# Performance work log

Hardware: AMD Instinct MI355X
Metric: run time of the kernel (lower is better)

Reference implementation:

```python
import jax, jax.numpy as jnp
import numpy as np

B, T = 1024, 1024
D_IN, UNITS, WIDTH, DEPTH, D_OUT = 6, 64, 128, 3, 6
START = UNITS + D_IN  # concat([x_normed, h]) width
EPS = 1e-8


def _xavier(key, fin, fout):
    lim = float(np.sqrt(6.0 / (fin + fout)))
    return jax.random.uniform(key, (fin, fout), minval=-lim, maxval=lim, dtype=jnp.float32)


def setup_inputs() -> dict:
    key = jax.random.key(0)
    ks = jax.random.split(key, 12)
    d = {
        "x": jax.random.normal(ks[0], (B, T, D_IN), dtype=jnp.float32),
        "init_F": jax.random.normal(ks[1], (B, 2 + UNITS), dtype=jnp.float32) * 0.1,
    }
    dims = [START] + [WIDTH] * DEPTH
    for i in range(DEPTH):
        d[f"qb1_w{i}"] = _xavier(ks[2 + 2 * i], dims[i], dims[i + 1])
        d[f"qb1_b{i}"] = jnp.zeros((dims[i + 1],), dtype=jnp.float32)
        d[f"qb2_w{i}"] = _xavier(ks[3 + 2 * i], dims[i], dims[i + 1])
        d[f"qb2_b{i}"] = jnp.zeros((dims[i + 1],), dtype=jnp.float32)
    d["wa"] = _xavier(ks[8], WIDTH, UNITS)
    d["ba"] = jnp.zeros((UNITS,), dtype=jnp.float32)
    d["wb"] = _xavier(ks[9], WIDTH, UNITS)
    d["bb"] = jnp.zeros((UNITS,), dtype=jnp.float32)
    # fc_out bias is frozen at zero in the original -> weight only
    d["wout"] = _xavier(ks[10], UNITS, D_OUT)
    return d


def reference(x, init_F,
              qb1_w0, qb1_b0, qb2_w0, qb2_b0,
              qb1_w1, qb1_b1, qb2_w1, qb2_b1,
              qb1_w2, qb1_b2, qb2_w2, qb2_b2,
              wa, ba, wb, bb, wout):
    layers = ((qb1_w0, qb1_b0, qb2_w0, qb2_b0),
              (qb1_w1, qb1_b1, qb2_w1, qb2_b1),
              (qb1_w2, qb1_b2, qb2_w2, qb2_b2))
    h0 = init_F[:, 2:2 + UNITS]  # [B, UNITS]

    def step(h, xt):  # xt: [B, D_IN], h: [B, UNITS]
        norm = jnp.sqrt(jnp.sum(xt * xt, axis=1, keepdims=True))  # [B,1]
        xn = xt / (norm + EPS)
        c = jnp.concatenate([xn, h], axis=1)  # [B, START]
        for i, (w1, b1, w2, b2) in enumerate(layers):
            x1 = c @ w1 + b1
            x2 = c @ w2 + b2
            if i < DEPTH - 1:
                x1 = jnp.tanh(x1)
                x2 = jnp.tanh(x2)
            c = x1 * x2
        g = jnp.tanh(c)
        alpha = jnp.exp(g @ wa + ba)          # [B, UNITS]
        beta = jnp.tanh(g @ wb + bb)          # [B, UNITS]
        h_new = jnp.exp(-alpha * norm) * (h - beta) + beta
        return h_new, (h_new @ wout, alpha)

    _, (outs, alphas) = jax.lax.scan(step, h0, jnp.swapaxes(x, 0, 1))
    # outs: [T,B,D_OUT], alphas: [T,B,UNITS] -> batch-major
    return jnp.swapaxes(outs, 0, 1), jnp.swapaxes(alphas, 0, 1)
```

## Files before the change

### kernel.cpp

```cpp
#include <hip/hip_runtime.h>
#include <stdint.h>
#include <stddef.h>

#define NB 1024
#define TB 1024
#define D_IN 6
#define UNITS 64
#define WIDTH 128
#define DOUT 6
#define EPSF 1e-8f
#define SPB 16
#define LDK0 108
#define LDK 140

typedef _Float16 v8h __attribute__((ext_vector_type(8)));
typedef float v4f __attribute__((ext_vector_type(4)));

#define MFMAH(A,Bf,C) __builtin_amdgcn_mfma_f32_16x16x32_f16((A),(Bf),(C),0,0,0)

#define BARRIER_LDS() asm volatile("s_waitcnt lgkmcnt(0)\n\ts_barrier" ::: "memory")

#define C2L2E  2.8853900817779268f
#define L2E    1.4426950408889634f
#define NEGL2E (-1.4426950408889634f)

__device__ __forceinline__ float rcp_fast(float x){ return __builtin_amdgcn_rcpf(x); }

__device__ __forceinline__ float tanh_from_arg(float a2){
  float u = __builtin_amdgcn_exp2f(a2);
  return fmaf(-2.0f, rcp_fast(u + 1.0f), 1.0f);
}
__device__ __forceinline__ float tanh_e(float x){ return tanh_from_arg(x * C2L2E); }

__device__ __forceinline__ void make_frag1(const float* vals, v8h& hv){
  #pragma unroll
  for (int j = 0; j < 8; j++) hv[j] = (_Float16)vals[j];
}
__device__ __forceinline__ void make_frag2(const float* vals, v8h& hv, v8h& lv){
  #pragma unroll
  for (int j = 0; j < 8; j++){
    _Float16 h = (_Float16)vals[j];
    hv[j] = h;
    lv[j] = (_Float16)(vals[j] - (float)h);
  }
}

__global__ __launch_bounds__(512, 2) void lmsc_kernel(
    const float* __restrict__ x, const float* __restrict__ initF,
    const float* __restrict__ w10, const float* __restrict__ b10,
    const float* __restrict__ w20, const float* __restrict__ b20,
    const float* __restrict__ w11, const float* __restrict__ b11,
    const float* __restrict__ w21, const float* __restrict__ b21,
    const float* __restrict__ w12, const float* __restrict__ b12,
    const float* __restrict__ w22, const float* __restrict__ b22,
    const float* __restrict__ wa, const float* __restrict__ ba,
    const float* __restrict__ wb, const float* __restrict__ bb,
    const float* __restrict__ wo,
    float* __restrict__ outs, float* __restrict__ alph)
{
  __shared__ __attribute__((aligned(16))) _Float16 c0[2][SPB*LDK0];
  __shared__ __attribute__((aligned(16))) _Float16 cP[SPB*LDK];
  __shared__ __attribute__((aligned(16))) _Float16 cQ[SPB*LDK];
  __shared__ __attribute__((aligned(16))) _Float16 cG[SPB*LDK];
  __shared__ __attribute__((aligned(16))) float nrm[2][SPB];

  const int tid = threadIdx.x;
  const int wv = tid >> 6;
  const int ln = tid & 63;
  const int mn = ln & 15;
  const int qd = ln >> 4;
  const int q8 = qd * 8;
  const int n  = wv * 16 + mn;
  const int sgbase = (int)blockIdx.x * SPB;

  float tmp[8];

  v8h B0[3][2];
  #pragma unroll
  for (int kf = 0; kf < 3; kf++)
    #pragma unroll
    for (int br = 0; br < 2; br++){
      const float* W = br ? w20 : w10;
      #pragma unroll
      for (int j = 0; j < 8; j++){
        int k = kf*32 + q8 + j;
        int r = (k < 6) ? k : ((k >= 8 && k < 72) ? (k - 2) : -1);
        tmp[j] = (r >= 0) ? W[r*WIDTH + n] : 0.0f;
      }
      make_frag1(tmp, B0[kf][br]);
    }

  v8h B1[4][2], B2[4][2];
  #pragma unroll
  for (int kf = 0; kf < 4; kf++)
    #pragma unroll
    for (int br = 0; br < 2; br++){
      const float* W = br ? w21 : w11;
      #pragma unroll
      for (int j = 0; j < 8; j++)
        tmp[j] = W[(kf*32 + q8 + j)*WIDTH + n];
      make_frag1(tmp, B1[kf][br]);
      const float* V = br ? w22 : w12;
      #pragma unroll
      for (int j = 0; j < 8; j++)
        tmp[j] = V[(kf*32 + q8 + j)*WIDTH + n];
      make_frag1(tmp, B2[kf][br]);
    }

  const int u = (wv & 3) * 16 + mn;
  v8h Bah[4], Bal[4], Bbh[4];
  #pragma unroll
  for (int kf = 0; kf < 4; kf++){
    #pragma unroll
    for (int j = 0; j < 8; j++)
      tmp[j] = wa[(kf*32 + q8 + j)*UNITS + u];
    make_frag2(tmp, Bah[kf], Bal[kf]);
    #pragma unroll
    for (int j = 0; j < 8; j++)
      tmp[j] = wb[(kf*32 + q8 + j)*UNITS + u];
    make_frag1(tmp, Bbh[kf]);
  }
  const float bsa = ba[u];
  const float bsb = bb[u];

  v8h Woh0, Woh1;
  #pragma unroll
  for (int j = 0; j < 8; j++)
    tmp[j] = (mn < DOUT) ? wo[(q8 + j)*DOUT + mn] : 0.0f;
  make_frag1(tmp, Woh0);
  #pragma unroll
  for (int j = 0; j < 8; j++)
    tmp[j] = (mn < DOUT) ? wo[(32 + q8 + j)*DOUT + mn] : 0.0f;
  make_frag1(tmp, Woh1);

  const float bs0a = b10[n], bs0b = b20[n];
  const float bs1a = b11[n], bs1b = b21[n];
  const float bs2a = b12[n], bs2b = b22[n];
  const float e0a = bs0a * C2L2E, e0b = bs0b * C2L2E;
  const float e1a = bs1a * C2L2E, e1b = bs1b * C2L2E;

  float* alp  = alph + ((size_t)(sgbase + qd*4) * TB) * UNITS + u;
  float* outp = outs + ((size_t)(sgbase + qd*4) * TB) * DOUT + mn;

  for (int i = tid; i < 2*SPB*LDK0; i += 512) c0[0][i] = (_Float16)0.0f;
  __syncthreads();

  float hreg[4];
  if (wv < 4){
    #pragma unroll
    for (int r = 0; r < 4; r++){
      int s = qd*4 + r;
      float v = initF[(size_t)(sgbase + s)*(2 + UNITS) + 2 + u];
      hreg[r] = v;
      c0[0][s*LDK0 + 8 + u] = (_Float16)v;
    }
  }
  float xv0=0, xv1=0, xv2=0, xv3=0, xv4=0, xv5=0;
  if (wv == 4 && ln < 16){
    const float* xp = x + (size_t)(sgbase + ln)*TB*D_IN;
    float a0=xp[0], a1=xp[1], a2=xp[2], a3=xp[3], a4=xp[4], a5=xp[5];
    float nv = sqrtf(a0*a0 + a1*a1 + a2*a2 + a3*a3 + a4*a4 + a5*a5);
    nrm[0][ln] = nv * NEGL2E;
    float inv = 1.0f / (nv + EPSF);
    c0[0][ln*LDK0 + 0] = (_Float16)(a0*inv);
    c0[0][ln*LDK0 + 1] = (_Float16)(a1*inv);
    c0[0][ln*LDK0 + 2] = (_Float16)(a2*inv);
    c0[0][ln*LDK0 + 3] = (_Float16)(a3*inv);
    c0[0][ln*LDK0 + 4] = (_Float16)(a4*inv);
    c0[0][ln*LDK0 + 5] = (_Float16)(a5*inv);
    xv0 = xp[6]; xv1 = xp[7]; xv2 = xp[8]; xv3 = xp[9]; xv4 = xp[10]; xv5 = xp[11];
  }
  __syncthreads();

  auto wout_phase = [&](const _Float16* cb, int tt){
    v8h ah0 = *(const v8h*)(cb + mn*LDK0 + 8 + q8);
    v8h ah1 = *(const v8h*)(cb + mn*LDK0 + 40 + q8);
    v4f acc = {0.f, 0.f, 0.f, 0.f};
    acc = MFMAH(ah0, Woh0, acc);
    acc = MFMAH(ah1, Woh1, acc);
    if (mn < DOUT){
      #pragma unroll
      for (int r = 0; r < 4; r++)
        outp[(size_t)r*TB*DOUT + (size_t)tt*DOUT] = acc[r];
    }
  };

  for (int t = 0; t < TB; t++){
    const int p = t & 1;
    const _Float16* c0r = c0[p];
    _Float16* c0w = c0[p ^ 1];

    {
      v8h ah[3];
      #pragma unroll
      for (int kf = 0; kf < 3; kf++)
        ah[kf] = *(const v8h*)(c0r + mn*LDK0 + kf*32 + q8);
      v4f acc0 = {0.f, 0.f, 0.f, 0.f};
      v4f acc1 = {0.f, 0.f, 0.f, 0.f};
      #pragma unroll
      for (int kf = 0; kf < 3; kf++){
        acc0 = MFMAH(ah[kf], B0[kf][0], acc0);
        acc1 = MFMAH(ah[kf], B0[kf][1], acc1);
      }
      #pragma unroll
      for (int r = 0; r < 4; r++){
        float t0 = tanh_from_arg(fmaf(acc0[r], C2L2E, e0a));
        float t1 = tanh_from_arg(fmaf(acc1[r], C2L2E, e0b));
        cP[(qd*4 + r)*LDK + n] = (_Float16)(t0 * t1);
      }
    }
    BARRIER_LDS();

    {
      v8h ah[4];
      #pragma unroll
      for (int kf = 0; kf < 4; kf++)
        ah[kf] = *(const v8h*)(cP + mn*LDK + kf*32 + q8);
      v4f acc0 = {0.f, 0.f, 0.f, 0.f};
      v4f acc1 = {0.f, 0.f, 0.f, 0.f};
      #pragma unroll
      for (int kf = 0; kf < 4; kf++){
        acc0 = MFMAH(ah[kf], B1[kf][0], acc0);
        acc1 = MFMAH(ah[kf], B1[kf][1], acc1);
      }
      #pragma unroll
      for (int r = 0; r < 4; r++){
        float t0 = tanh_from_arg(fmaf(acc0[r], C2L2E, e1a));
        float t1 = tanh_from_arg(fmaf(acc1[r], C2L2E, e1b));
        cQ[(qd*4 + r)*LDK + n] = (_Float16)(t0 * t1);
      }
    }
    BARRIER_LDS();

    {
      v8h ah[4];
      #pragma unroll
      for (int kf = 0; kf < 4; kf++)
        ah[kf] = *(const v8h*)(cQ + mn*LDK + kf*32 + q8);
      v4f acc0 = {bs2a, bs2a, bs2a, bs2a};
      v4f acc1 = {bs2b, bs2b, bs2b, bs2b};
      #pragma unroll
      for (int kf = 0; kf < 4; kf++){
        acc0 = MFMAH(ah[kf], B2[kf][0], acc0);
        acc1 = MFMAH(ah[kf], B2[kf][1], acc1);
      }
      #pragma unroll
      for (int r = 0; r < 4; r++)
        cG[(qd*4 + r)*LDK + n] = (_Float16)tanh_e(acc0[r] * acc1[r]);
    }
    BARRIER_LDS();

    if (wv < 4){
      v8h gh[4];
      #pragma unroll
      for (int kf = 0; kf < 4; kf++)
        gh[kf] = *(const v8h*)(cG + mn*LDK + kf*32 + q8);
      v4f pA0 = {bsa, bsa, bsa, bsa};
      v4f pA1 = {0.f, 0.f, 0.f, 0.f};
      v4f pB  = {bsb, bsb, bsb, bsb};
      #pragma unroll
      for (int kf = 0; kf < 2; kf++){
        pA0 = MFMAH(gh[kf], Bah[kf], pA0);
        pA0 = MFMAH(gh[kf], Bal[kf], pA0);
        pA1 = MFMAH(gh[kf+2], Bah[kf+2], pA1);
        pA1 = MFMAH(gh[kf+2], Bal[kf+2], pA1);
        pB  = MFMAH(gh[2*kf],   Bbh[2*kf],   pB);
        pB  = MFMAH(gh[2*kf+1], Bbh[2*kf+1], pB);
      }
      #pragma unroll
      for (int r = 0; r < 4; r++){
        int s = qd*4 + r;
        float m = nrm[p][s];
        float alpha = __builtin_amdgcn_exp2f((pA0[r] + pA1[r]) * L2E);
        float beta  = tanh_e(pB[r]);
        float dec   = __builtin_amdgcn_exp2f(alpha * m);
        float h = fmaf(dec, hreg[r] - beta, beta);
        hreg[r] = h;
        c0w[s*LDK0 + 8 + u] = (_Float16)h;
        alp[(size_t)r*TB*UNITS] = alpha;
      }
      alp += UNITS;
    } else if (wv == 7){
      if (t > 0) wout_phase(c0r, t - 1);
    } else if (wv == 4 && ln < 16){
      float nv2 = sqrtf(xv0*xv0 + xv1*xv1 + xv2*xv2 + xv3*xv3 + xv4*xv4 + xv5*xv5);
      nrm[p ^ 1][ln] = nv2 * NEGL2E;
      float inv = 1.0f / (nv2 + EPSF);
      c0w[ln*LDK0 + 0] = (_Float16)(xv0*inv);
      c0w[ln*LDK0 + 1] = (_Float16)(xv1*inv);
      c0w[ln*LDK0 + 2] = (_Float16)(xv2*inv);
      c0w[ln*LDK0 + 3] = (_Float16)(xv3*inv);
      c0w[ln*LDK0 + 4] = (_Float16)(xv4*inv);
      c0w[ln*LDK0 + 5] = (_Float16)(xv5*inv);
      int tn = t + 2; if (tn > TB - 1) tn = TB - 1;
      const float* xp = x + ((size_t)(sgbase + ln)*TB + (size_t)tn)*D_IN;
      xv0 = xp[0]; xv1 = xp[1]; xv2 = xp[2]; xv3 = xp[3]; xv4 = xp[4]; xv5 = xp[5];
    }
    BARRIER_LDS();
  }

  if (wv == 7) wout_phase(c0[TB & 1], TB - 1);
}

extern "C" void kernel_launch(void* const* d_in, const int* in_sizes, int n_in,
                              void* d_out, int out_size, void* d_ws, size_t ws_size,
                              hipStream_t stream) {
  const float* x    = (const float*)d_in[0];
  const float* iF   = (const float*)d_in[1];
  const float* w10  = (const float*)d_in[2];
  const float* b10  = (const float*)d_in[3];
  const float* w20  = (const float*)d_in[4];
  const float* b20  = (const float*)d_in[5];
  const float* w11  = (const float*)d_in[6];
  const float* b11  = (const float*)d_in[7];
  const float* w21  = (const float*)d_in[8];
  const float* b21  = (const float*)d_in[9];
  const float* w12  = (const float*)d_in[10];
  const float* b12  = (const float*)d_in[11];
  const float* w22  = (const float*)d_in[12];
  const float* b22  = (const float*)d_in[13];
  const float* wa   = (const float*)d_in[14];
  const float* ba   = (const float*)d_in[15];
  const float* wb   = (const float*)d_in[16];
  const float* bb   = (const float*)d_in[17];
  const float* wo   = (const float*)d_in[18];

  float* outs = (float*)d_out;
  float* alph = outs + (size_t)NB*TB*DOUT;

  lmsc_kernel<<<NB/SPB, 512, 0, stream>>>(x, iF,
      w10, b10, w20, b20, w11, b11, w21, b21, w12, b12, w22, b22,
      wa, ba, wb, bb, wo, outs, alph);
}
```

Before: 2.379 ms.

## Process two 16-sequence tiles per block, sharing weight fragments across tiles

Doubles sequences per block from 16 to 32 by splitting the block's state into two 16-row tiles. Every wave now runs interleaved MFMA chains for both tiles against the same register-resident weight fragments. All eight waves take part in the alpha/beta/h update phase, and the output projection is split between waves 1 and 6. The aim is to hide per-step MFMA and barrier latency with independent work and to reuse weights. The cost is half as many blocks on an already underfilled GPU, and roughly twice the work on each block's serial time-step path.

```diff
diff --git a/kernel.cpp b/kernel.cpp
--- a/kernel.cpp
+++ b/kernel.cpp
@@ -9,7 +9,8 @@
 #define WIDTH 128
 #define DOUT 6
 #define EPSF 1e-8f
-#define SPB 16
+#define SPB 32
+#define T16 16
 #define LDK0 108
 #define LDK 140
 
@@ -58,11 +59,11 @@
     const float* __restrict__ wo,
     float* __restrict__ outs, float* __restrict__ alph)
 {
-  __shared__ __attribute__((aligned(16))) _Float16 c0[2][SPB*LDK0];
-  __shared__ __attribute__((aligned(16))) _Float16 cP[SPB*LDK];
-  __shared__ __attribute__((aligned(16))) _Float16 cQ[SPB*LDK];
-  __shared__ __attribute__((aligned(16))) _Float16 cG[SPB*LDK];
-  __shared__ __attribute__((aligned(16))) float nrm[2][SPB];
+  __shared__ __attribute__((aligned(16))) _Float16 c0[2][2][T16*LDK0];
+  __shared__ __attribute__((aligned(16))) _Float16 cP[2][T16*LDK];
+  __shared__ __attribute__((aligned(16))) _Float16 cQ[2][T16*LDK];
+  __shared__ __attribute__((aligned(16))) _Float16 cG[2][T16*LDK];
+  __shared__ __attribute__((aligned(16))) float nrm[2][2][T16];
 
   const int tid = threadIdx.x;
   const int wv = tid >> 6;
@@ -72,6 +73,7 @@
   const int q8 = qd * 8;
   const int n  = wv * 16 + mn;
   const int sgbase = (int)blockIdx.x * SPB;
+  const int dtile = wv >> 2;
 
   float tmp[8];
 
@@ -133,41 +135,44 @@
     tmp[j] = (mn < DOUT) ? wo[(32 + q8 + j)*DOUT + mn] : 0.0f;
   make_frag1(tmp, Woh1);
 
-  const float bs0a = b10[n], bs0b = b20[n];
-  const float bs1a = b11[n], bs1b = b21[n];
   const float bs2a = b12[n], bs2b = b22[n];
-  const float e0a = bs0a * C2L2E, e0b = bs0b * C2L2E;
-  const float e1a = bs1a * C2L2E, e1b = bs1b * C2L2E;
-
-  float* alp  = alph + ((size_t)(sgbase + qd*4) * TB) * UNITS + u;
-  float* outp = outs + ((size_t)(sgbase + qd*4) * TB) * DOUT + mn;
-
-  for (int i = tid; i < 2*SPB*LDK0; i += 512) c0[0][i] = (_Float16)0.0f;
+  const float e0a = b10[n] * C2L2E, e0b = b20[n] * C2L2E;
+  const float e1a = b11[n] * C2L2E, e1b = b21[n] * C2L2E;
+
+  float* alp  = alph + ((size_t)(sgbase + dtile*T16 + qd*4) * TB) * UNITS + u;
+  const int wtile = (wv == 1) ? 0 : 1;
+  float* outp = outs + ((size_t)(sgbase + wtile*T16 + qd*4) * TB) * DOUT + mn;
+
+  {
+    _Float16* cz = &c0[0][0][0];
+    for (int i = tid; i < 2*2*T16*LDK0; i += 512) cz[i] = (_Float16)0.0f;
+  }
   __syncthreads();
 
   float hreg[4];
-  if (wv < 4){
-    #pragma unroll
-    for (int r = 0; r < 4; r++){
-      int s = qd*4 + r;
-      float v = initF[(size_t)(sgbase + s)*(2 + UNITS) + 2 + u];
-      hreg[r] = v;
-      c0[0][s*LDK0 + 8 + u] = (_Float16)v;
-    }
-  }
+  #pragma unroll
+  for (int r = 0; r < 4; r++){
+    int s = qd*4 + r;
+    float v = initF[(size_t)(sgbase + dtile*T16 + s)*(2 + UNITS) + 2 + u];
+    hreg[r] = v;
+    c0[0][dtile][s*LDK0 + 8 + u] = (_Float16)v;
+  }
+
   float xv0=0, xv1=0, xv2=0, xv3=0, xv4=0, xv5=0;
-  if (wv == 4 && ln < 16){
+  if (wv == 4 && ln < 32){
+    const int tl = ln >> 4, s = ln & 15;
     const float* xp = x + (size_t)(sgbase + ln)*TB*D_IN;
     float a0=xp[0], a1=xp[1], a2=xp[2], a3=xp[3], a4=xp[4], a5=xp[5];
     float nv = sqrtf(a0*a0 + a1*a1 + a2*a2 + a3*a3 + a4*a4 + a5*a5);
-    nrm[0][ln] = nv * NEGL2E;
+    nrm[0][tl][s] = nv * NEGL2E;
     float inv = 1.0f / (nv + EPSF);
-    c0[0][ln*LDK0 + 0] = (_Float16)(a0*inv);
-    c0[0][ln*LDK0 + 1] = (_Float16)(a1*inv);
-    c0[0][ln*LDK0 + 2] = (_Float16)(a2*inv);
-    c0[0][ln*LDK0 + 3] = (_Float16)(a3*inv);
-    c0[0][ln*LDK0 + 4] = (_Float16)(a4*inv);
-    c0[0][ln*LDK0 + 5] = (_Float16)(a5*inv);
+    _Float16* cw = &c0[0][tl][0];
+    cw[s*LDK0 + 0] = (_Float16)(a0*inv);
+    cw[s*LDK0 + 1] = (_Float16)(a1*inv);
+    cw[s*LDK0 + 2] = (_Float16)(a2*inv);
+    cw[s*LDK0 + 3] = (_Float16)(a3*inv);
+    cw[s*LDK0 + 4] = (_Float16)(a4*inv);
+    cw[s*LDK0 + 5] = (_Float16)(a5*inv);
     xv0 = xp[6]; xv1 = xp[7]; xv2 = xp[8]; xv3 = xp[9]; xv4 = xp[10]; xv5 = xp[11];
   }
   __syncthreads();
@@ -187,74 +192,95 @@
 
   for (int t = 0; t < TB; t++){
     const int p = t & 1;
-    const _Float16* c0r = c0[p];
-    _Float16* c0w = c0[p ^ 1];
+    const _Float16* c0r0 = c0[p][0];
+    const _Float16* c0r1 = c0[p][1];
+    _Float16* c0w0 = c0[p ^ 1][0];
+    _Float16* c0w1 = c0[p ^ 1][1];
 
     {
-      v8h ah[3];
-      #pragma unroll
-      for (int kf = 0; kf < 3; kf++)
-        ah[kf] = *(const v8h*)(c0r + mn*LDK0 + kf*32 + q8);
-      v4f acc0 = {0.f, 0.f, 0.f, 0.f};
-      v4f acc1 = {0.f, 0.f, 0.f, 0.f};
+      v8h a0[3], a1[3];
       #pragma unroll
       for (int kf = 0; kf < 3; kf++){
-        acc0 = MFMAH(ah[kf], B0[kf][0], acc0);
-        acc1 = MFMAH(ah[kf], B0[kf][1], acc1);
+        a0[kf] = *(const v8h*)(c0r0 + mn*LDK0 + kf*32 + q8);
+        a1[kf] = *(const v8h*)(c0r1 + mn*LDK0 + kf*32 + q8);
+      }
+      v4f q00 = {0,0,0,0}, q01 = {0,0,0,0}, q10 = {0,0,0,0}, q11 = {0,0,0,0};
+      #pragma unroll
+      for (int kf = 0; kf < 3; kf++){
+        q00 = MFMAH(a0[kf], B0[kf][0], q00);
+        q01 = MFMAH(a0[kf], B0[kf][1], q01);
+        q10 = MFMAH(a1[kf], B0[kf][0], q10);
+        q11 = MFMAH(a1[kf], B0[kf][1], q11);
       }
       #pragma unroll
       for (int r = 0; r < 4; r++){
-        float t0 = tanh_from_arg(fmaf(acc0[r], C2L2E, e0a));
-        float t1 = tanh_from_arg(fmaf(acc1[r], C2L2E, e0b));
-        cP[(qd*4 + r)*LDK + n] = (_Float16)(t0 * t1);
+        float t0 = tanh_from_arg(fmaf(q00[r], C2L2E, e0a));
+        float t1 = tanh_from_arg(fmaf(q01[r], C2L2E, e0b));
+        cP[0][(qd*4 + r)*LDK + n] = (_Float16)(t0 * t1);
+        float s0 = tanh_from_arg(fmaf(q10[r], C2L2E, e0a));
+        float s1 = tanh_from_arg(fmaf(q11[r], C2L2E, e0b));
+        cP[1][(qd*4 + r)*LDK + n] = (_Float16)(s0 * s1);
       }
     }
     BARRIER_LDS();
 
     {
-      v8h ah[4];
+      v8h a0[4], a1[4];
+      #pragma unroll
+      for (int kf = 0; kf < 4; kf++){
+        a0[kf] = *(const v8h*)(cP[0] + mn*LDK + kf*32 + q8);
+        a1[kf] = *(const v8h*)(cP[1] + mn*LDK + kf*32 + q8);
+      }
+      v4f q00 = {0,0,0,0}, q01 = {0,0,0,0}, q10 = {0,0,0,0}, q11 = {0,0,0,0};
+      #pragma unroll
+      for (int kf = 0; kf < 4; kf++){
+        q00 = MFMAH(a0[kf], B1[kf][0], q00);
+        q01 = MFMAH(a0[kf], B1[kf][1], q01);
+        q10 = MFMAH(a1[kf], B1[kf][0], q10);
+        q11 = MFMAH(a1[kf], B1[kf][1], q11);
+      }
+      #pragma unroll
+      for (int r = 0; r < 4; r++){
+        float t0 = tanh_from_arg(fmaf(q00[r], C2L2E, e1a));
+        float t1 = tanh_from_arg(fmaf(q01[r], C2L2E, e1b));
+        cQ[0][(qd*4 + r)*LDK + n] = (_Float16)(t0 * t1);
+        float s0 = tanh_from_arg(fmaf(q10[r], C2L2E, e1a));
+        float s1 = tanh_from_arg(fmaf(q11[r], C2L2E, e1b));
+        cQ[1][(qd*4 + r)*LDK + n] = (_Float16)(s0 * s1);
+      }
+    }
+    BARRIER_LDS();
+
+    {
+      v8h a0[4], a1[4];
+      #pragma unroll
+      for (int kf = 0; kf < 4; kf++){
+        a0[kf] = *(const v8h*)(cQ[0] + mn*LDK + kf*32 + q8);
+        a1[kf] = *(const v8h*)(cQ[1] + mn*LDK + kf*32 + q8);
+      }
+      v4f q00 = {bs2a,bs2a,bs2a,bs2a}, q01 = {bs2b,bs2b,bs2b,bs2b};
+      v4f q10 = {bs2a,bs2a,bs2a,bs2a}, q11 = {bs2b,bs2b,bs2b,bs2b};
+      #pragma unroll
+      for (int kf = 0; kf < 4; kf++){
+        q00 = MFMAH(a0[kf], B2[kf][0], q00);
+        q01 = MFMAH(a0[kf], B2[kf][1], q01);
+        q10 = MFMAH(a1[kf], B2[kf][0], q10);
+        q11 = MFMAH(a1[kf], B2[kf][1], q11);
+      }
+      #pragma unroll
+      for (int r = 0; r < 4; r++){
+        cG[0][(qd*4 + r)*LDK + n] = (_Float16)tanh_e(q00[r] * q01[r]);
+        cG[1][(qd*4 + r)*LDK + n] = (_Float16)tanh_e(q10[r] * q11[r]);
+      }
+    }
+    BARRIER_LDS();
+
+    {
+      const _Float16* cGt = cG[dtile];
+      v8h gh[4];
       #pragma unroll
       for (int kf = 0; kf < 4; kf++)
-        ah[kf] = *(const v8h*)(cP + mn*LDK + kf*32 + q8);
-      v4f acc0 = {0.f, 0.f, 0.f, 0.f};
-      v4f acc1 = {0.f, 0.f, 0.f, 0.f};
-      #pragma unroll
-      for (int kf = 0; kf < 4; kf++){
-        acc0 = MFMAH(ah[kf], B1[kf][0], acc0);
-        acc1 = MFMAH(ah[kf], B1[kf][1], acc1);
-      }
-      #pragma unroll
-      for (int r = 0; r < 4; r++){
-        float t0 = tanh_from_arg(fmaf(acc0[r], C2L2E, e1a));
-        float t1 = tanh_from_arg(fmaf(acc1[r], C2L2E, e1b));
-        cQ[(qd*4 + r)*LDK + n] = (_Float16)(t0 * t1);
-      }
-    }
-    BARRIER_LDS();
-
-    {
-      v8h ah[4];
-      #pragma unroll
-      for (int kf = 0; kf < 4; kf++)
-        ah[kf] = *(const v8h*)(cQ + mn*LDK + kf*32 + q8);
-      v4f acc0 = {bs2a, bs2a, bs2a, bs2a};
-      v4f acc1 = {bs2b, bs2b, bs2b, bs2b};
-      #pragma unroll
-      for (int kf = 0; kf < 4; kf++){
-        acc0 = MFMAH(ah[kf], B2[kf][0], acc0);
-        acc1 = MFMAH(ah[kf], B2[kf][1], acc1);
-      }
-      #pragma unroll
-      for (int r = 0; r < 4; r++)
-        cG[(qd*4 + r)*LDK + n] = (_Float16)tanh_e(acc0[r] * acc1[r]);
-    }
-    BARRIER_LDS();
-
-    if (wv < 4){
-      v8h gh[4];
-      #pragma unroll
-      for (int kf = 0; kf < 4; kf++)
-        gh[kf] = *(const v8h*)(cG + mn*LDK + kf*32 + q8);
+        gh[kf] = *(const v8h*)(cGt + mn*LDK + kf*32 + q8);
       v4f pA0 = {bsa, bsa, bsa, bsa};
       v4f pA1 = {0.f, 0.f, 0.f, 0.f};
       v4f pB  = {bsb, bsb, bsb, bsb};
@@ -267,31 +293,38 @@
         pB  = MFMAH(gh[2*kf],   Bbh[2*kf],   pB);
         pB  = MFMAH(gh[2*kf+1], Bbh[2*kf+1], pB);
       }
+      _Float16* c0wt = dtile ? c0w1 : c0w0;
+      const float* nr = nrm[p][dtile];
       #pragma unroll
       for (int r = 0; r < 4; r++){
         int s = qd*4 + r;
-        float m = nrm[p][s];
+        float m = nr[s];
         float alpha = __builtin_amdgcn_exp2f((pA0[r] + pA1[r]) * L2E);
         float beta  = tanh_e(pB[r]);
         float dec   = __builtin_amdgcn_exp2f(alpha * m);
         float h = fmaf(dec, hreg[r] - beta, beta);
         hreg[r] = h;
-        c0w[s*LDK0 + 8 + u] = (_Float16)h;
+        c0wt[s*LDK0 + 8 + u] = (_Float16)h;
         alp[(size_t)r*TB*UNITS] = alpha;
       }
       alp += UNITS;
-    } else if (wv == 7){
-      if (t > 0) wout_phase(c0r, t - 1);
-    } else if (wv == 4 && ln < 16){
+    }
+    if (wv == 1){
+      if (t > 0) wout_phase(c0r0, t - 1);
+    } else if (wv == 6){
+      if (t > 0) wout_phase(c0r1, t - 1);
+    } else if (wv == 4 && ln < 32){
+      const int tl = ln >> 4, s = ln & 15;
       float nv2 = sqrtf(xv0*xv0 + xv1*xv1 + xv2*xv2 + xv3*xv3 + xv4*xv4 + xv5*xv5);
-      nrm[p ^ 1][ln] = nv2 * NEGL2E;
+      nrm[p ^ 1][tl][s] = nv2 * NEGL2E;
       float inv = 1.0f / (nv2 + EPSF);
-      c0w[ln*LDK0 + 0] = (_Float16)(xv0*inv);
-      c0w[ln*LDK0 + 1] = (_Float16)(xv1*inv);
-      c0w[ln*LDK0 + 2] = (_Float16)(xv2*inv);
-      c0w[ln*LDK0 + 3] = (_Float16)(xv3*inv);
-      c0w[ln*LDK0 + 4] = (_Float16)(xv4*inv);
-      c0w[ln*LDK0 + 5] = (_Float16)(xv5*inv);
+      _Float16* cw = tl ? c0w1 : c0w0;
+      cw[s*LDK0 + 0] = (_Float16)(xv0*inv);
+      cw[s*LDK0 + 1] = (_Float16)(xv1*inv);
+      cw[s*LDK0 + 2] = (_Float16)(xv2*inv);
+      cw[s*LDK0 + 3] = (_Float16)(xv3*inv);
+      cw[s*LDK0 + 4] = (_Float16)(xv4*inv);
+      cw[s*LDK0 + 5] = (_Float16)(xv5*inv);
       int tn = t + 2; if (tn > TB - 1) tn = TB - 1;
       const float* xp = x + ((size_t)(sgbase + ln)*TB + (size_t)tn)*D_IN;
       xv0 = xp[0]; xv1 = xp[1]; xv2 = xp[2]; xv3 = xp[3]; xv4 = xp[4]; xv5 = xp[5];
@@ -299,7 +332,8 @@
     BARRIER_LDS();
   }
 
-  if (wv == 7) wout_phase(c0[TB & 1], TB - 1);
+  if (wv == 1) wout_phase(&c0[TB & 1][0][0], TB - 1);
+  else if (wv == 6) wout_phase(&c0[TB & 1][1][0], TB - 1);
 }
 
 extern "C" void kernel_launch(void* const* d_in, const int* in_sizes, int n_in,
```

Result: slower. 4.893 ms (+105.7%).

## Split warps into MLP-layer and gate/output roles with per-wave doubled columns

Applied to the files above, without the earlier changes.

Waves 0-3 now compute all three 128-wide MLP layers, each owning two 16-column groups. Waves 4-7 handle the alpha/beta gate, the state update, the x prefetch and the output projection. The aim is to take per-wave work off the serial critical chain and keep weights register-resident for each role only. The trade-off is that only half the waves do MFMA in the MLP stages, which doubles the serial MFMA chain per wave there. The state/input side-work is also rearranged around a barrier.

```diff
diff --git a/kernel.cpp b/kernel.cpp
--- a/kernel.cpp
+++ b/kernel.cpp
@@ -70,74 +70,82 @@
   const int mn = ln & 15;
   const int qd = ln >> 4;
   const int q8 = qd * 8;
-  const int n  = wv * 16 + mn;
   const int sgbase = (int)blockIdx.x * SPB;
 
+  const bool role_abc = (wv < 4);
+  const int n0 = wv * 16 + mn;
+  const int n1 = n0 + 64;
+  const int u  = (wv & 3) * 16 + mn;
+
   float tmp[8];
 
-  v8h B0[3][2];
-  #pragma unroll
-  for (int kf = 0; kf < 3; kf++)
+  v8h F0[12], F1[16], F2[16];
+  float EB[12];
+
+  if (role_abc){
     #pragma unroll
-    for (int br = 0; br < 2; br++){
-      const float* W = br ? w20 : w10;
-      #pragma unroll
-      for (int j = 0; j < 8; j++){
-        int k = kf*32 + q8 + j;
-        int r = (k < 6) ? k : ((k >= 8 && k < 72) ? (k - 2) : -1);
-        tmp[j] = (r >= 0) ? W[r*WIDTH + n] : 0.0f;
-      }
-      make_frag1(tmp, B0[kf][br]);
-    }
-
-  v8h B1[4][2], B2[4][2];
-  #pragma unroll
-  for (int kf = 0; kf < 4; kf++)
+    for (int g = 0; g < 2; g++){
+      const int nc = g ? n1 : n0;
+      #pragma unroll
+      for (int kf = 0; kf < 3; kf++)
+        #pragma unroll
+        for (int br = 0; br < 2; br++){
+          const float* W = br ? w20 : w10;
+          #pragma unroll
+          for (int j = 0; j < 8; j++){
+            int k = kf*32 + q8 + j;
+            int r = (k < 6) ? k : ((k >= 8 && k < 72) ? (k - 2) : -1);
+            tmp[j] = (r >= 0) ? W[r*WIDTH + nc] : 0.0f;
+          }
+          make_frag1(tmp, F0[g*6 + kf*2 + br]);
+        }
+      #pragma unroll
+      for (int kf = 0; kf < 4; kf++)
+        #pragma unroll
+        for (int br = 0; br < 2; br++){
+          const float* W = br ? w21 : w11;
+          #pragma unroll
+          for (int j = 0; j < 8; j++)
+            tmp[j] = W[(kf*32 + q8 + j)*WIDTH + nc];
+          make_frag1(tmp, F1[g*8 + kf*2 + br]);
+          const float* V = br ? w22 : w12;
+          #pragma unroll
+          for (int j = 0; j < 8; j++)
+            tmp[j] = V[(kf*32 + q8 + j)*WIDTH + nc];
+          make_frag1(tmp, F2[g*8 + kf*2 + br]);
+        }
+      EB[g*2 + 0] = b10[nc] * C2L2E;
+      EB[g*2 + 1] = b20[nc] * C2L2E;
+      EB[4 + g*2 + 0] = b11[nc] * C2L2E;
+      EB[4 + g*2 + 1] = b21[nc] * C2L2E;
+      EB[8 + g*2 + 0] = b12[nc];
+      EB[8 + g*2 + 1] = b22[nc];
+    }
+  } else {
     #pragma unroll
-    for (int br = 0; br < 2; br++){
-      const float* W = br ? w21 : w11;
+    for (int kf = 0; kf < 4; kf++){
       #pragma unroll
       for (int j = 0; j < 8; j++)
-        tmp[j] = W[(kf*32 + q8 + j)*WIDTH + n];
-      make_frag1(tmp, B1[kf][br]);
-      const float* V = br ? w22 : w12;
+        tmp[j] = wa[(kf*32 + q8 + j)*UNITS + u];
+      make_frag2(tmp, F0[kf], F0[4 + kf]);
       #pragma unroll
       for (int j = 0; j < 8; j++)
-        tmp[j] = V[(kf*32 + q8 + j)*WIDTH + n];
-      make_frag1(tmp, B2[kf][br]);
-    }
-
-  const int u = (wv & 3) * 16 + mn;
-  v8h Bah[4], Bal[4], Bbh[4];
-  #pragma unroll
-  for (int kf = 0; kf < 4; kf++){
-    #pragma unroll
-    for (int j = 0; j < 8; j++)
-      tmp[j] = wa[(kf*32 + q8 + j)*UNITS + u];
-    make_frag2(tmp, Bah[kf], Bal[kf]);
-    #pragma unroll
-    for (int j = 0; j < 8; j++)
-      tmp[j] = wb[(kf*32 + q8 + j)*UNITS + u];
-    make_frag1(tmp, Bbh[kf]);
-  }
-  const float bsa = ba[u];
-  const float bsb = bb[u];
-
-  v8h Woh0, Woh1;
-  #pragma unroll
-  for (int j = 0; j < 8; j++)
-    tmp[j] = (mn < DOUT) ? wo[(q8 + j)*DOUT + mn] : 0.0f;
-  make_frag1(tmp, Woh0);
-  #pragma unroll
-  for (int j = 0; j < 8; j++)
-    tmp[j] = (mn < DOUT) ? wo[(32 + q8 + j)*DOUT + mn] : 0.0f;
-  make_frag1(tmp, Woh1);
-
-  const float bs0a = b10[n], bs0b = b20[n];
-  const float bs1a = b11[n], bs1b = b21[n];
-  const float bs2a = b12[n], bs2b = b22[n];
-  const float e0a = bs0a * C2L2E, e0b = bs0b * C2L2E;
-  const float e1a = bs1a * C2L2E, e1b = bs1b * C2L2E;
+        tmp[j] = wb[(kf*32 + q8 + j)*UNITS + u];
+      make_frag1(tmp, F0[8 + kf]);
+    }
+    EB[0] = ba[u];
+    EB[1] = bb[u];
+    if (wv == 6){
+      #pragma unroll
+      for (int j = 0; j < 8; j++)
+        tmp[j] = (mn < DOUT) ? wo[(q8 + j)*DOUT + mn] : 0.0f;
+      make_frag1(tmp, F1[0]);
+      #pragma unroll
+      for (int j = 0; j < 8; j++)
+        tmp[j] = (mn < DOUT) ? wo[(32 + q8 + j)*DOUT + mn] : 0.0f;
+      make_frag1(tmp, F1[1]);
+    }
+  }
 
   float* alp  = alph + ((size_t)(sgbase + qd*4) * TB) * UNITS + u;
   float* outp = outs + ((size_t)(sgbase + qd*4) * TB) * DOUT + mn;
@@ -146,7 +154,7 @@
   __syncthreads();
 
   float hreg[4];
-  if (wv < 4){
+  if (!role_abc){
     #pragma unroll
     for (int r = 0; r < 4; r++){
       int s = qd*4 + r;
@@ -156,7 +164,7 @@
     }
   }
   float xv0=0, xv1=0, xv2=0, xv3=0, xv4=0, xv5=0;
-  if (wv == 4 && ln < 16){
+  if (wv == 5 && ln < 16){
     const float* xp = x + (size_t)(sgbase + ln)*TB*D_IN;
     float a0=xp[0], a1=xp[1], a2=xp[2], a3=xp[3], a4=xp[4], a5=xp[5];
     float nv = sqrtf(a0*a0 + a1*a1 + a2*a2 + a3*a3 + a4*a4 + a5*a5);
@@ -176,8 +184,8 @@
     v8h ah0 = *(const v8h*)(cb + mn*LDK0 + 8 + q8);
     v8h ah1 = *(const v8h*)(cb + mn*LDK0 + 40 + q8);
     v4f acc = {0.f, 0.f, 0.f, 0.f};
-    acc = MFMAH(ah0, Woh0, acc);
-    acc = MFMAH(ah1, Woh1, acc);
+    acc = MFMAH(ah0, F1[0], acc);
+    acc = MFMAH(ah1, F1[1], acc);
     if (mn < DOUT){
       #pragma unroll
       for (int r = 0; r < 4; r++)
@@ -190,99 +198,96 @@
     const _Float16* c0r = c0[p];
     _Float16* c0w = c0[p ^ 1];
 
-    {
+    if (role_abc){
       v8h ah[3];
       #pragma unroll
       for (int kf = 0; kf < 3; kf++)
         ah[kf] = *(const v8h*)(c0r + mn*LDK0 + kf*32 + q8);
-      v4f acc0 = {0.f, 0.f, 0.f, 0.f};
-      v4f acc1 = {0.f, 0.f, 0.f, 0.f};
-      #pragma unroll
-      for (int kf = 0; kf < 3; kf++){
-        acc0 = MFMAH(ah[kf], B0[kf][0], acc0);
-        acc1 = MFMAH(ah[kf], B0[kf][1], acc1);
-      }
+      v4f ac[2][2];
+      #pragma unroll
+      for (int g = 0; g < 2; g++)
+        #pragma unroll
+        for (int br = 0; br < 2; br++)
+          ac[g][br] = (v4f){0.f, 0.f, 0.f, 0.f};
+      #pragma unroll
+      for (int kf = 0; kf < 3; kf++)
+        #pragma unroll
+        for (int g = 0; g < 2; g++){
+          ac[g][0] = MFMAH(ah[kf], F0[g*6 + kf*2 + 0], ac[g][0]);
+          ac[g][1] = MFMAH(ah[kf], F0[g*6 + kf*2 + 1], ac[g][1]);
+        }
       #pragma unroll
       for (int r = 0; r < 4; r++){
-        float t0 = tanh_from_arg(fmaf(acc0[r], C2L2E, e0a));
-        float t1 = tanh_from_arg(fmaf(acc1[r], C2L2E, e0b));
-        cP[(qd*4 + r)*LDK + n] = (_Float16)(t0 * t1);
+        const int row = (qd*4 + r)*LDK;
+        #pragma unroll
+        for (int g = 0; g < 2; g++){
+          float t0 = tanh_from_arg(fmaf(ac[g][0][r], C2L2E, EB[g*2 + 0]));
+          float t1 = tanh_from_arg(fmaf(ac[g][1][r], C2L2E, EB[g*2 + 1]));
+          cP[row + (g ? n1 : n0)] = (_Float16)(t0 * t1);
+        }
       }
     }
     BARRIER_LDS();
 
-    {
+    if (role_abc){
       v8h ah[4];
       #pragma unroll
       for (int kf = 0; kf < 4; kf++)
         ah[kf] = *(const v8h*)(cP + mn*LDK + kf*32 + q8);
-      v4f acc0 = {0.f, 0.f, 0.f, 0.f};
-      v4f acc1 = {0.f, 0.f, 0.f, 0.f};
-      #pragma unroll
-      for (int kf = 0; kf < 4; kf++){
-        acc0 = MFMAH(ah[kf], B1[kf][0], acc0);
-        acc1 = MFMAH(ah[kf], B1[kf][1], acc1);
-      }
+      v4f ac[2][2];
+      #pragma unroll
+      for (int g = 0; g < 2; g++)
+        #pragma unroll
+        for (int br = 0; br < 2; br++)
+          ac[g][br] = (v4f){0.f, 0.f, 0.f, 0.f};
+      #pragma unroll
+      for (int kf = 0; kf < 4; kf++)
+        #pragma unroll
+        for (int g = 0; g < 2; g++){
+          ac[g][0] = MFMAH(ah[kf], F1[g*8 + kf*2 + 0], ac[g][0]);
+          ac[g][1] = MFMAH(ah[kf], F1[g*8 + kf*2 + 1], ac[g][1]);
+        }
       #pragma unroll
       for (int r = 0; r < 4; r++){
-        float t0 = tanh_from_arg(fmaf(acc0[r], C2L2E, e1a));
-        float t1 = tanh_from_arg(fmaf(acc1[r], C2L2E, e1b));
-        cQ[(qd*4 + r)*LDK + n] = (_Float16)(t0 * t1);
+        const int row = (qd*4 + r)*LDK;
+        #pragma unroll
+        for (int g = 0; g < 2; g++){
+          float t0 = tanh_from_arg(fmaf(ac[g][0][r], C2L2E, EB[4 + g*2 + 0]));
+          float t1 = tanh_from_arg(fmaf(ac[g][1][r], C2L2E, EB[4 + g*2 + 1]));
+          cQ[row + (g ? n1 : n0)] = (_Float16)(t0 * t1);
+        }
       }
     }
     BARRIER_LDS();
 
-    {
+    if (role_abc){
       v8h ah[4];
       #pragma unroll
       for (int kf = 0; kf < 4; kf++)
         ah[kf] = *(const v8h*)(cQ + mn*LDK + kf*32 + q8);
-      v4f acc0 = {bs2a, bs2a, bs2a, bs2a};
-      v4f acc1 = {bs2b, bs2b, bs2b, bs2b};
-      #pragma unroll
-      for (int kf = 0; kf < 4; kf++){
-        acc0 = MFMAH(ah[kf], B2[kf][0], acc0);
-        acc1 = MFMAH(ah[kf], B2[kf][1], acc1);
-      }
-      #pragma unroll
-      for (int r = 0; r < 4; r++)
-        cG[(qd*4 + r)*LDK + n] = (_Float16)tanh_e(acc0[r] * acc1[r]);
-    }
-    BARRIER_LDS();
-
-    if (wv < 4){
-      v8h gh[4];
-      #pragma unroll
-      for (int kf = 0; kf < 4; kf++)
-        gh[kf] = *(const v8h*)(cG + mn*LDK + kf*32 + q8);
-      v4f pA0 = {bsa, bsa, bsa, bsa};
-      v4f pA1 = {0.f, 0.f, 0.f, 0.f};
-      v4f pB  = {bsb, bsb, bsb, bsb};
-      #pragma unroll
-      for (int kf = 0; kf < 2; kf++){
-        pA0 = MFMAH(gh[kf], Bah[kf], pA0);
-        pA0 = MFMAH(gh[kf], Bal[kf], pA0);
-        pA1 = MFMAH(gh[kf+2], Bah[kf+2], pA1);
-        pA1 = MFMAH(gh[kf+2], Bal[kf+2], pA1);
-        pB  = MFMAH(gh[2*kf],   Bbh[2*kf],   pB);
-        pB  = MFMAH(gh[2*kf+1], Bbh[2*kf+1], pB);
-      }
+      v4f ac[2][2];
+      #pragma unroll
+      for (int g = 0; g < 2; g++)
+        #pragma unroll
+        for (int br = 0; br < 2; br++){
+          float b = EB[8 + g*2 + br];
+          ac[g][br] = (v4f){b, b, b, b};
+        }
+      #pragma unroll
+      for (int kf = 0; kf < 4; kf++)
+        #pragma unroll
+        for (int g = 0; g < 2; g++){
+          ac[g][0] = MFMAH(ah[kf], F2[g*8 + kf*2 + 0], ac[g][0]);
+          ac[g][1] = MFMAH(ah[kf], F2[g*8 + kf*2 + 1], ac[g][1]);
+        }
       #pragma unroll
       for (int r = 0; r < 4; r++){
-        int s = qd*4 + r;
-        float m = nrm[p][s];
-        float alpha = __builtin_amdgcn_exp2f((pA0[r] + pA1[r]) * L2E);
-        float beta  = tanh_e(pB[r]);
-        float dec   = __builtin_amdgcn_exp2f(alpha * m);
-        float h = fmaf(dec, hreg[r] - beta, beta);
-        hreg[r] = h;
-        c0w[s*LDK0 + 8 + u] = (_Float16)h;
-        alp[(size_t)r*TB*UNITS] = alpha;
-      }
-      alp += UNITS;
-    } else if (wv == 7){
-      if (t > 0) wout_phase(c0r, t - 1);
-    } else if (wv == 4 && ln < 16){
+        const int row = (qd*4 + r)*LDK;
+        #pragma unroll
+        for (int g = 0; g < 2; g++)
+          cG[row + (g ? n1 : n0)] = (_Float16)tanh_e(ac[g][0][r] * ac[g][1][r]);
+      }
+    } else if (wv == 5 && ln < 16){
       float nv2 = sqrtf(xv0*xv0 + xv1*xv1 + xv2*xv2 + xv3*xv3 + xv4*xv4 + xv5*xv5);
       nrm[p ^ 1][ln] = nv2 * NEGL2E;
       float inv = 1.0f / (nv2 + EPSF);
@@ -295,11 +300,46 @@
       int tn = t + 2; if (tn > TB - 1) tn = TB - 1;
       const float* xp = x + ((size_t)(sgbase + ln)*TB + (size_t)tn)*D_IN;
       xv0 = xp[0]; xv1 = xp[1]; xv2 = xp[2]; xv3 = xp[3]; xv4 = xp[4]; xv5 = xp[5];
+    } else if (wv == 6){
+      if (t > 0) wout_phase(c0r, t - 1);
     }
     BARRIER_LDS();
-  }
-
-  if (wv == 7) wout_phase(c0[TB & 1], TB - 1);
+
+    if (!role_abc){
+      v8h gh[4];
+      #pragma unroll
+      for (int kf = 0; kf < 4; kf++)
+        gh[kf] = *(const v8h*)(cG + mn*LDK + kf*32 + q8);
+      v4f pA0 = {EB[0], EB[0], EB[0], EB[0]};
+      v4f pA1 = {0.f, 0.f, 0.f, 0.f};
+      v4f pB  = {EB[1], EB[1], EB[1], EB[1]};
+      #pragma unroll
+      for (int kf = 0; kf < 2; kf++){
+        pA0 = MFMAH(gh[kf],   F0[kf],       pA0);
+        pA0 = MFMAH(gh[kf],   F0[4 + kf],   pA0);
+        pA1 = MFMAH(gh[kf+2], F0[kf + 2],   pA1);
+        pA1 = MFMAH(gh[kf+2], F0[6 + kf],   pA1);
+        pB  = MFMAH(gh[2*kf],   F0[8 + 2*kf],   pB);
+        pB  = MFMAH(gh[2*kf+1], F0[8 + 2*kf+1], pB);
+      }
+      #pragma unroll
+      for (int r = 0; r < 4; r++){
+        int s = qd*4 + r;
+        float m = nrm[p][s];
+        float alpha = __builtin_amdgcn_exp2f((pA0[r] + pA1[r]) * L2E);
+        float beta  = tanh_e(pB[r]);
+        float dec   = __builtin_amdgcn_exp2f(alpha * m);
+        float h = fmaf(dec, hreg[r] - beta, beta);
+        hreg[r] = h;
+        c0w[s*LDK0 + 8 + u] = (_Float16)h;
+        alp[(size_t)r*TB*UNITS] = alpha;
+      }
+      alp += UNITS;
+    }
+    BARRIER_LDS();
+  }
+
+  if (wv == 6) wout_phase(c0[0], TB - 1);
 }
 
 extern "C" void kernel_launch(void* const* d_in, const int* in_sizes, int n_in,
```

Result: slower. 2.710 ms (+13.9%).
